# Optimization experiments

Hardware: AMD Instinct MI355X
Metric: run time of the kernel (lower is better)

## Reference

```python
import jax, jax.numpy as jnp
import numpy as np

B, N, M, C, H = 8, 1024, 128, 1024, 16
D = C // H
MLP = int(C * 4.0)
EPS = 1e-6


def setup_inputs() -> dict:
    key = jax.random.key(0)
    ks = jax.random.split(key, 24)
    def w(k, shape):
        return jax.random.normal(k, shape, jnp.float32) * 0.02
    mask = jax.random.randint(ks[3], (B, M), 0, 2, dtype=jnp.int32)
    mask = mask.at[:, 0].set(1)  # ensure at least one attendable token per row
    return {
        "x": jax.random.normal(ks[0], (B, N, C), jnp.float32),
        "c_dino": jax.random.normal(ks[1], (B, C), jnp.float32),
        "c_text": jax.random.normal(ks[2], (B, M, C), jnp.float32),
        "text_mask": mask,
        "W_ada": w(ks[4], (C, 6 * C)), "b_ada": jnp.zeros((6 * C,), jnp.float32),
        "W_qkv": w(ks[5], (C, 3 * C)), "b_qkv": jnp.zeros((3 * C,), jnp.float32),
        "W_proj_sa": w(ks[6], (C, C)), "b_proj_sa": jnp.zeros((C,), jnp.float32),
        "W_q": w(ks[7], (C, C)), "b_q": jnp.zeros((C,), jnp.float32),
        "W_kv": w(ks[8], (C, 2 * C)), "b_kv": jnp.zeros((2 * C,), jnp.float32),
        "W_proj_ca": w(ks[9], (C, C)), "b_proj_ca": jnp.zeros((C,), jnp.float32),
        "W_fc1": w(ks[10], (C, MLP)), "b_fc1": jnp.zeros((MLP,), jnp.float32),
        "W_fc2": w(ks[11], (MLP, C)), "b_fc2": jnp.zeros((C,), jnp.float32),
    }


def _ln(x):
    # LayerNorm without affine params, eps=1e-6
    mu = jnp.mean(x, axis=-1, keepdims=True)
    xc = x - mu
    var = jnp.mean(xc * xc, axis=-1, keepdims=True)
    return xc * jax.lax.rsqrt(var + EPS)


def _modulate(x, shift, scale):
    return x * (1.0 + scale[:, None, :]) + shift[:, None, :]


def _heads(t):
    b, n, _ = t.shape
    return t.reshape(b, n, H, D)


def reference(x, c_dino, c_text, text_mask,
              W_ada, b_ada, W_qkv, b_qkv, W_proj_sa, b_proj_sa,
              W_q, b_q, W_kv, b_kv, W_proj_ca, b_proj_ca,
              W_fc1, b_fc1, W_fc2, b_fc2):
    scale = D ** (-0.5)
    ada = jax.nn.silu(c_dino) @ W_ada + b_ada  # (B, 6C)
    sh_msa, sc_msa, sh_ca, sc_ca, sh_mlp, sc_mlp = jnp.split(ada, 6, axis=1)

    # --- self-attention ---
    h = _modulate(_ln(x), sh_msa, sc_msa)
    qkv = h @ W_qkv + b_qkv
    q, k, v = (_heads(t) for t in jnp.split(qkv, 3, axis=-1))  # (B,N,H,D)
    attn = jax.nn.softmax(jnp.einsum('bnhd,bmhd->bhnm', q, k) * scale, axis=-1)
    sa = jnp.einsum('bhnm,bmhd->bnhd', attn, v).reshape(B, N, C) @ W_proj_sa + b_proj_sa
    x = x + sa

    # --- cross-attention ---
    h = _modulate(_ln(x), sh_ca, sc_ca)
    q = _heads(h @ W_q + b_q)                 # (B,N,H,D)
    kv = c_text @ W_kv + b_kv
    k, v = (_heads(t) for t in jnp.split(kv, 2, axis=-1))  # (B,M,H,D)
    scores = jnp.einsum('bnhd,bmhd->bhnm', q, k) * scale
    scores = jnp.where(text_mask[:, None, None, :] == 0, -jnp.inf, scores)
    attn = jax.nn.softmax(scores, axis=-1)
    ca = jnp.einsum('bhnm,bmhd->bnhd', attn, v).reshape(B, N, C) @ W_proj_ca + b_proj_ca
    x = x + ca

    # --- MLP ---
    h = _modulate(_ln(x), sh_mlp, sc_mlp)
    mlp = jax.nn.gelu(h @ W_fc1 + b_fc1, approximate=True) @ W_fc2 + b_fc2
    return x + mlp
```

## Files before the change

### kernel.cpp

```cpp
#include <hip/hip_runtime.h>
#include <hip/hip_bf16.h>

#define B_   8
#define N_   1024
#define M_   128
#define C_   1024
#define H_   16
#define D_   64
#define MLP_ 4096

typedef __bf16 bf16;
typedef __bf16 bf16x8 __attribute__((ext_vector_type(8)));
typedef __bf16 bf16x4 __attribute__((ext_vector_type(4)));
typedef float  f32x4  __attribute__((ext_vector_type(4)));

__device__ __forceinline__ f32x4 mfma16(bf16x8 a, bf16x8 b, f32x4 c) {
    return __builtin_amdgcn_mfma_f32_16x16x32_bf16(a, b, c, 0, 0, 0);
}

__device__ __forceinline__ void gload16(const bf16* g, bf16* l) {
    __builtin_amdgcn_global_load_lds(
        (const __attribute__((address_space(1))) void*)g,
        (__attribute__((address_space(3))) void*)l, 16, 0, 0);
}

__global__ __launch_bounds__(256) void transpose_k(const float* __restrict__ W,
                                                   bf16* __restrict__ Wt,
                                                   int K, int Nc) {
    __shared__ float tile[32][33];
    const int x  = threadIdx.x & 31;
    const int y0 = threadIdx.x >> 5;
    const size_t n0 = (size_t)blockIdx.x * 32;
    const size_t k0 = (size_t)blockIdx.y * 32;
#pragma unroll
    for (int i = 0; i < 4; i++)
        tile[y0 + i * 8][x] = W[(k0 + y0 + i * 8) * Nc + n0 + x];
    __syncthreads();
#pragma unroll
    for (int i = 0; i < 4; i++)
        Wt[(n0 + y0 + i * 8) * K + k0 + x] = (bf16)tile[x][y0 + i * 8];
}

__global__ __launch_bounds__(256) void cvt_bf16_k(const float* __restrict__ in,
                                                  bf16* __restrict__ out, int n4) {
    int i = blockIdx.x * 256 + threadIdx.x;
    if (i < n4) {
        float4 v = ((const float4*)in)[i];
        bf16x4 o;
        o[0] = (bf16)v.x; o[1] = (bf16)v.y; o[2] = (bf16)v.z; o[3] = (bf16)v.w;
        ((bf16x4*)out)[i] = o;
    }
}

__global__ __launch_bounds__(256) void ada_init_k(const float* __restrict__ bias,
                                                  float* __restrict__ ada) {
    int i = blockIdx.x * 256 + threadIdx.x;
    ada[i] = bias[i % 6144];
}

__global__ __launch_bounds__(256) void ada_k(const float* __restrict__ cdino,
                                             const float* __restrict__ W,
                                             float* __restrict__ ada) {
    __shared__ float sc[8][32];
    const int tid = threadIdx.x;
    const int k0  = blockIdx.y * 32;
    {
        float c = cdino[(tid >> 5) * 1024 + k0 + (tid & 31)];
        sc[tid >> 5][tid & 31] = c / (1.f + __expf(-c));
    }
    __syncthreads();
    const int col = blockIdx.x * 256 + tid;
    float acc[8];
#pragma unroll
    for (int b = 0; b < 8; b++) acc[b] = 0.f;
    for (int kk = 0; kk < 32; kk++) {
        float w = W[(size_t)(k0 + kk) * 6144 + col];
#pragma unroll
        for (int b = 0; b < 8; b++) acc[b] += sc[b][kk] * w;
    }
#pragma unroll
    for (int b = 0; b < 8; b++) atomicAdd(&ada[(size_t)b * 6144 + col], acc[b]);
}

__global__ __launch_bounds__(256) void ln_mod_k(const float* __restrict__ X,
                                                const float* __restrict__ ada,
                                                int shoff, int scoff,
                                                bf16* __restrict__ Hout) {
    const int row = blockIdx.x;
    const int b   = row >> 10;
    const int tid = threadIdx.x;
    const float4 v = ((const float4*)(X + (size_t)row * C_))[tid];
    float s  = v.x + v.y + v.z + v.w;
    float sq = v.x * v.x + v.y * v.y + v.z * v.z + v.w * v.w;
#pragma unroll
    for (int off = 32; off; off >>= 1) {
        s  += __shfl_xor(s,  off);
        sq += __shfl_xor(sq, off);
    }
    __shared__ float rs_[4], rq_[4];
    if ((tid & 63) == 0) { rs_[tid >> 6] = s; rq_[tid >> 6] = sq; }
    __syncthreads();
    s  = rs_[0] + rs_[1] + rs_[2] + rs_[3];
    sq = rq_[0] + rq_[1] + rq_[2] + rq_[3];
    const float mu   = s * (1.f / 1024.f);
    const float var  = sq * (1.f / 1024.f) - mu * mu;
    const float rstd = rsqrtf(var + 1e-6f);
    const float4 scv = ((const float4*)(ada + (size_t)b * 6144 + scoff))[tid];
    const float4 shv = ((const float4*)(ada + (size_t)b * 6144 + shoff))[tid];
    bf16x4 o;
    o[0] = (bf16)(((v.x - mu) * rstd) * (1.f + scv.x) + shv.x);
    o[1] = (bf16)(((v.y - mu) * rstd) * (1.f + scv.y) + shv.y);
    o[2] = (bf16)(((v.z - mu) * rstd) * (1.f + scv.z) + shv.z);
    o[3] = (bf16)(((v.w - mu) * rstd) * (1.f + scv.w) + shv.w);
    *(bf16x4*)(Hout + (size_t)row * C_ + tid * 4) = o;
}

template <int MODE>
__global__ __launch_bounds__(256) void gemm_k(const bf16* __restrict__ A,
                                              const bf16* __restrict__ Bt,
                                              const float* __restrict__ bias,
                                              const float* resid,
                                              float* outF, bf16* outB,
                                              int Ncols, int K) {
    __shared__ __attribute__((aligned(16))) bf16 As[128][32];
    __shared__ __attribute__((aligned(16))) bf16 Bs[128][32];
    const int tid  = threadIdx.x;
    const int lane = tid & 63, wave = tid >> 6;
    const int lrow = lane & 15, quad = lane >> 4;
    const int wm = wave >> 1, wn = wave & 1;
    const size_t bm = (size_t)blockIdx.y * 128;
    const size_t bn = (size_t)blockIdx.x * 128;

    const int srow = tid >> 2, sseg = tid & 3;
    const bf16* gA0 = A  + (bm + srow) * (size_t)K + sseg * 8;
    const bf16* gA1 = gA0 + (size_t)64 * K;
    const bf16* gB0 = Bt + (bn + srow) * (size_t)K + sseg * 8;
    const bf16* gB1 = gB0 + (size_t)64 * K;
    bf16* lA0 = &As[0][0] + wave * 512;
    bf16* lA1 = lA0 + 2048;
    bf16* lB0 = &Bs[0][0] + wave * 512;
    bf16* lB1 = lB0 + 2048;

    f32x4 acc[4][4];
#pragma unroll
    for (int i = 0; i < 4; i++)
#pragma unroll
        for (int j = 0; j < 4; j++) acc[i][j] = (f32x4){0.f, 0.f, 0.f, 0.f};

    for (int ko = 0; ko < K; ko += 32) {
        gload16(gA0 + ko, lA0);
        gload16(gA1 + ko, lA1);
        gload16(gB0 + ko, lB0);
        gload16(gB1 + ko, lB1);
        __syncthreads();
        bf16x8 af[4], bfr[4];
#pragma unroll
        for (int mi = 0; mi < 4; mi++)
            af[mi] = *(const bf16x8*)&As[wm * 64 + mi * 16 + lrow][quad * 8];
#pragma unroll
        for (int ni = 0; ni < 4; ni++)
            bfr[ni] = *(const bf16x8*)&Bs[wn * 64 + ni * 16 + lrow][quad * 8];
#pragma unroll
        for (int mi = 0; mi < 4; mi++)
#pragma unroll
            for (int ni = 0; ni < 4; ni++)
                acc[mi][ni] = mfma16(af[mi], bfr[ni], acc[mi][ni]);
        __syncthreads();
    }

#pragma unroll
    for (int mi = 0; mi < 4; mi++) {
#pragma unroll
        for (int ni = 0; ni < 4; ni++) {
            const size_t gcol = bn + wn * 64 + ni * 16 + lrow;
            const float bv = bias[gcol];
#pragma unroll
            for (int r = 0; r < 4; r++) {
                const size_t grow = bm + wm * 64 + mi * 16 + quad * 4 + r;
                const size_t idx  = grow * Ncols + gcol;
                float v = acc[mi][ni][r] + bv;
                if (MODE == 1) {
                    outF[idx] = v + resid[idx];
                } else if (MODE == 2) {
                    outB[idx] = (bf16)v;
                } else {
                    float z = 1.59576912f * (v + 0.044715f * v * v * v);
                    outB[idx] = (bf16)(v / (1.f + __expf(-z)));
                }
            }
        }
    }
}

template <bool MASKED>
__global__ __launch_bounds__(256) void attn_k(const bf16* __restrict__ Qp, int qstride,
                                              const bf16* __restrict__ KVp, int kvstride,
                                              int koff, int voff,
                                              const int* __restrict__ mask, int Mk,
                                              bf16* __restrict__ O) {
    __shared__ __attribute__((aligned(16))) bf16 Kt[64][88];
    __shared__ __attribute__((aligned(16))) bf16 Vt[64][88];
    __shared__ __attribute__((aligned(16))) bf16 Pt[4][16][88];
    __shared__ float madd[64];

    const int b = blockIdx.z, h = blockIdx.y;
    const int tid  = threadIdx.x;
    const int lane = tid & 63, wave = tid >> 6;
    const int lrow = lane & 15, quad = lane >> 4;
    const int q0 = blockIdx.x * 64 + wave * 16;

    const bf16* qp = Qp + ((size_t)(b * N_ + q0 + lrow)) * qstride + h * 64 + quad * 8;
    const bf16x8 aq0 = *(const bf16x8*)(qp);
    const bf16x8 aq1 = *(const bf16x8*)(qp + 32);

    f32x4 acc[4];
#pragma unroll
    for (int t = 0; t < 4; t++) acc[t] = (f32x4){0.f, 0.f, 0.f, 0.f};
    float mrun[4], lrun[4];
#pragma unroll
    for (int r = 0; r < 4; r++) { mrun[r] = -3e38f; lrun[r] = 0.f; }

    const int skey = tid >> 2;
    const int sd   = (tid & 3) * 16;

    for (int kc = 0; kc < Mk; kc += 64) {
        __syncthreads();
        const bf16* kp = KVp + ((size_t)(b * Mk + kc + skey)) * kvstride + koff + h * 64 + sd;
        bf16x8 k0 = *(const bf16x8*)kp;
        bf16x8 k1 = *(const bf16x8*)(kp + 8);
        *(bf16x8*)&Kt[skey][sd]     = k0;
        *(bf16x8*)&Kt[skey][sd + 8] = k1;
        const bf16* vp = KVp + ((size_t)(b * Mk + kc + skey)) * kvstride + voff + h * 64 + sd;
        bf16x8 v0 = *(const bf16x8*)vp;
        bf16x8 v1 = *(const bf16x8*)(vp + 8);
#pragma unroll
        for (int i = 0; i < 8; i++) Vt[sd + i][skey] = v0[i];
#pragma unroll
        for (int i = 0; i < 8; i++) Vt[sd + 8 + i][skey] = v1[i];
        if (MASKED && tid < 64)
            madd[tid] = (mask[b * Mk + kc + tid] == 0) ? -1e30f : 0.f;
        __syncthreads();

        float sv[4][4];
#pragma unroll
        for (int t = 0; t < 4; t++) {
            f32x4 s = (f32x4){0.f, 0.f, 0.f, 0.f};
            bf16x8 bk0 = *(const bf16x8*)&Kt[t * 16 + lrow][quad * 8];
            s = mfma16(aq0, bk0, s);
            bf16x8 bk1 = *(const bf16x8*)&Kt[t * 16 + lrow][32 + quad * 8];
            s = mfma16(aq1, bk1, s);
            const float ma = MASKED ? madd[t * 16 + lrow] : 0.f;
#pragma unroll
            for (int r = 0; r < 4; r++) sv[t][r] = s[r] * 0.125f + ma;
        }

        float pv[4][4], alpha[4];
#pragma unroll
        for (int r = 0; r < 4; r++) {
            float vmax = fmaxf(fmaxf(sv[0][r], sv[1][r]), fmaxf(sv[2][r], sv[3][r]));
#pragma unroll
            for (int off = 1; off < 16; off <<= 1) vmax = fmaxf(vmax, __shfl_xor(vmax, off));
            const float mnew = fmaxf(mrun[r], vmax);
            alpha[r] = __expf(mrun[r] - mnew);
            mrun[r] = mnew;
            float rsum = 0.f;
#pragma unroll
            for (int t = 0; t < 4; t++) {
                float p = __expf(sv[t][r] - mnew);
                pv[t][r] = p;
                rsum += p;
            }
#pragma unroll
            for (int off = 1; off < 16; off <<= 1) rsum += __shfl_xor(rsum, off);
            lrun[r] = lrun[r] * alpha[r] + rsum;
        }
#pragma unroll
        for (int t = 0; t < 4; t++)
#pragma unroll
            for (int r = 0; r < 4; r++) acc[t][r] *= alpha[r];

#pragma unroll
        for (int t = 0; t < 4; t++)
#pragma unroll
            for (int r = 0; r < 4; r++)
                Pt[wave][quad * 4 + r][t * 16 + lrow] = (bf16)pv[t][r];
        __syncthreads();
        const bf16x8 ap0 = *(const bf16x8*)&Pt[wave][lrow][quad * 8];
        const bf16x8 ap1 = *(const bf16x8*)&Pt[wave][lrow][32 + quad * 8];

#pragma unroll
        for (int t = 0; t < 4; t++) {
            bf16x8 bv0 = *(const bf16x8*)&Vt[t * 16 + lrow][quad * 8];
            acc[t] = mfma16(ap0, bv0, acc[t]);
            bf16x8 bv1 = *(const bf16x8*)&Vt[t * 16 + lrow][32 + quad * 8];
            acc[t] = mfma16(ap1, bv1, acc[t]);
        }
    }

#pragma unroll
    for (int r = 0; r < 4; r++) {
        const float inv = 1.f / lrun[r];
        const size_t grow = (size_t)(b * N_ + q0 + quad * 4 + r);
#pragma unroll
        for (int t = 0; t < 4; t++)
            O[grow * C_ + h * 64 + t * 16 + lrow] = (bf16)(acc[t][r] * inv);
    }
}

extern "C" void kernel_launch(void* const* d_in, const int* in_sizes, int n_in,
                              void* d_out, int out_size, void* d_ws, size_t ws_size,
                              hipStream_t stream) {
    const float* x     = (const float*)d_in[0];
    const float* cdino = (const float*)d_in[1];
    const float* ctext = (const float*)d_in[2];
    const int*   tmask = (const int*)d_in[3];
    const float* W_ada = (const float*)d_in[4];
    const float* b_ada = (const float*)d_in[5];
    const float* W_qkv = (const float*)d_in[6];
    const float* b_qkv = (const float*)d_in[7];
    const float* W_sa  = (const float*)d_in[8];
    const float* b_sa  = (const float*)d_in[9];
    const float* W_q   = (const float*)d_in[10];
    const float* b_q   = (const float*)d_in[11];
    const float* W_kv  = (const float*)d_in[12];
    const float* b_kv  = (const float*)d_in[13];
    const float* W_ca  = (const float*)d_in[14];
    const float* b_ca  = (const float*)d_in[15];
    const float* W_fc1 = (const float*)d_in[16];
    const float* b_fc1 = (const float*)d_in[17];
    const float* W_fc2 = (const float*)d_in[18];
    const float* b_fc2 = (const float*)d_in[19];
    float* out = (float*)d_out;

    char* ws = (char*)d_ws;
    size_t off = 0;
    auto alloc = [&](size_t bytes) -> char* {
        char* p = ws + off;
        off += (bytes + 255) & ~(size_t)255;
        return p;
    };
    float* ada  = (float*)alloc((size_t)8 * 6144 * 4);
    bf16* ctxb  = (bf16*)alloc((size_t)1024 * 1024 * 2);
    bf16* WqkvT = (bf16*)alloc((size_t)3072 * 1024 * 2);
    bf16* WsaT  = (bf16*)alloc((size_t)1024 * 1024 * 2);
    bf16* WqT   = (bf16*)alloc((size_t)1024 * 1024 * 2);
    bf16* WkvT  = (bf16*)alloc((size_t)2048 * 1024 * 2);
    bf16* WcaT  = (bf16*)alloc((size_t)1024 * 1024 * 2);
    bf16* Wfc1T = (bf16*)alloc((size_t)4096 * 1024 * 2);
    bf16* Wfc2T = (bf16*)alloc((size_t)1024 * 4096 * 2);
    float* xbuf = (float*)alloc((size_t)8192 * 1024 * 4);
    bf16* hbuf  = (bf16*)alloc((size_t)8192 * 1024 * 2);
    bf16* attnb = (bf16*)alloc((size_t)8192 * 1024 * 2);
    bf16* pool  = (bf16*)alloc((size_t)8192 * 4096 * 2);
    if (off > ws_size) return;

    bf16* qkvb  = pool;
    bf16* qb    = pool;
    bf16* kvb   = pool + (size_t)8192 * 1024;
    bf16* gelub = pool;

    transpose_k<<<dim3(3072 / 32, 1024 / 32), 256, 0, stream>>>(W_qkv, WqkvT, 1024, 3072);
    transpose_k<<<dim3(1024 / 32, 1024 / 32), 256, 0, stream>>>(W_sa,  WsaT,  1024, 1024);
    transpose_k<<<dim3(1024 / 32, 1024 / 32), 256, 0, stream>>>(W_q,   WqT,   1024, 1024);
    transpose_k<<<dim3(2048 / 32, 1024 / 32), 256, 0, stream>>>(W_kv,  WkvT,  1024, 2048);
    transpose_k<<<dim3(1024 / 32, 1024 / 32), 256, 0, stream>>>(W_ca,  WcaT,  1024, 1024);
    transpose_k<<<dim3(4096 / 32, 1024 / 32), 256, 0, stream>>>(W_fc1, Wfc1T, 1024, 4096);
    transpose_k<<<dim3(1024 / 32, 4096 / 32), 256, 0, stream>>>(W_fc2, Wfc2T, 4096, 1024);
    cvt_bf16_k<<<1024, 256, 0, stream>>>(ctext, ctxb, 262144);

    ada_init_k<<<192, 256, 0, stream>>>(b_ada, ada);
    ada_k<<<dim3(24, 32), 256, 0, stream>>>(cdino, W_ada, ada);

    ln_mod_k<<<8192, 256, 0, stream>>>(x, ada, 0, 1024, hbuf);
    gemm_k<2><<<dim3(24, 64), 256, 0, stream>>>(hbuf, WqkvT, b_qkv, nullptr, nullptr, qkvb, 3072, 1024);
    attn_k<false><<<dim3(16, 16, 8), 256, 0, stream>>>(qkvb, 3072, qkvb, 3072, 1024, 2048,
                                                       nullptr, 1024, attnb);
    gemm_k<1><<<dim3(8, 64), 256, 0, stream>>>(attnb, WsaT, b_sa, x, xbuf, nullptr, 1024, 1024);

    ln_mod_k<<<8192, 256, 0, stream>>>(xbuf, ada, 2048, 3072, hbuf);
    gemm_k<2><<<dim3(8, 64), 256, 0, stream>>>(hbuf, WqT, b_q, nullptr, nullptr, qb, 1024, 1024);
    gemm_k<2><<<dim3(16, 8), 256, 0, stream>>>(ctxb, WkvT, b_kv, nullptr, nullptr, kvb, 2048, 1024);
    attn_k<true><<<dim3(16, 16, 8), 256, 0, stream>>>(qb, 1024, kvb, 2048, 0, 1024,
                                                      tmask, 128, attnb);
    gemm_k<1><<<dim3(8, 64), 256, 0, stream>>>(attnb, WcaT, b_ca, xbuf, xbuf, nullptr, 1024, 1024);

    ln_mod_k<<<8192, 256, 0, stream>>>(xbuf, ada, 4096, 5120, hbuf);
    gemm_k<3><<<dim3(32, 64), 256, 0, stream>>>(hbuf, Wfc1T, b_fc1, nullptr, nullptr, gelub, 4096, 1024);
    gemm_k<1><<<dim3(8, 64), 256, 0, stream>>>(gelub, Wfc2T, b_fc2, xbuf, out, nullptr, 1024, 4096);
}
```

Baseline: 825.3 us.

## Pre-transpose V in global memory and compute transposed scores in attention

Adds a separate kernel that transposes V per batch into a head-dim-major global buffer, so the attention kernel can stage V into shared memory with vector stores instead of scattered scalar transposing writes. The score MFMA is also swapped to compute K·Q^T. Each lane then holds one query's scores across four rows, which shrinks the row max and sum reductions to two cross-lane shuffles. Probabilities are written to shared memory as packed bf16x4. This costs extra launches and an additional global write and read of V, in exchange for cheaper shared-memory staging and softmax inside attention.

```diff
diff --git a/kernel.cpp b/kernel.cpp
--- a/kernel.cpp
+++ b/kernel.cpp
@@ -39,6 +39,23 @@
 #pragma unroll
     for (int i = 0; i < 4; i++)
         Wt[(n0 + y0 + i * 8) * K + k0 + x] = (bf16)tile[x][y0 + i * 8];
+}
+
+__global__ __launch_bounds__(256) void vtrans_k(const bf16* __restrict__ in, int instride,
+                                                int coff, int Mk, bf16* __restrict__ outT) {
+    __shared__ bf16 t[32][33];
+    const int tx = threadIdx.x & 31;
+    const int ty0 = threadIdx.x >> 5;
+    const int m0  = blockIdx.x * 32;
+    const int hd0 = blockIdx.y * 32;
+    const int b   = blockIdx.z;
+#pragma unroll
+    for (int i = 0; i < 4; i++)
+        t[ty0 + i * 8][tx] = in[((size_t)(b * Mk + m0 + ty0 + i * 8)) * instride + coff + hd0 + tx];
+    __syncthreads();
+#pragma unroll
+    for (int i = 0; i < 4; i++)
+        outT[((size_t)(b * 1024 + hd0 + ty0 + i * 8)) * Mk + m0 + tx] = t[tx][ty0 + i * 8];
 }
 
 __global__ __launch_bounds__(256) void cvt_bf16_k(const float* __restrict__ in,
@@ -194,8 +211,8 @@
 
 template <bool MASKED>
 __global__ __launch_bounds__(256) void attn_k(const bf16* __restrict__ Qp, int qstride,
-                                              const bf16* __restrict__ KVp, int kvstride,
-                                              int koff, int voff,
+                                              const bf16* __restrict__ Kp, int kstride,
+                                              const bf16* __restrict__ Vtg,
                                               const int* __restrict__ mask, int Mk,
                                               bf16* __restrict__ O) {
     __shared__ __attribute__((aligned(16))) bf16 Kt[64][88];
@@ -210,33 +227,32 @@
     const int q0 = blockIdx.x * 64 + wave * 16;
 
     const bf16* qp = Qp + ((size_t)(b * N_ + q0 + lrow)) * qstride + h * 64 + quad * 8;
-    const bf16x8 aq0 = *(const bf16x8*)(qp);
-    const bf16x8 aq1 = *(const bf16x8*)(qp + 32);
+    const bf16x8 bq0 = *(const bf16x8*)(qp);
+    const bf16x8 bq1 = *(const bf16x8*)(qp + 32);
 
     f32x4 acc[4];
 #pragma unroll
     for (int t = 0; t < 4; t++) acc[t] = (f32x4){0.f, 0.f, 0.f, 0.f};
-    float mrun[4], lrun[4];
-#pragma unroll
-    for (int r = 0; r < 4; r++) { mrun[r] = -3e38f; lrun[r] = 0.f; }
-
-    const int skey = tid >> 2;
-    const int sd   = (tid & 3) * 16;
+    float mrun = -3e38f, lrun = 0.f;
+
+    const int srow = tid >> 2;
+    const int sseg = (tid & 3) * 16;
+
+    const bf16* kbase = Kp + ((size_t)b * Mk + srow) * kstride + h * 64 + sseg;
+    const bf16* vbase = Vtg + ((size_t)(b * 1024 + h * 64 + srow)) * Mk + sseg;
 
     for (int kc = 0; kc < Mk; kc += 64) {
         __syncthreads();
-        const bf16* kp = KVp + ((size_t)(b * Mk + kc + skey)) * kvstride + koff + h * 64 + sd;
+        const bf16* kp = kbase + (size_t)kc * kstride;
         bf16x8 k0 = *(const bf16x8*)kp;
         bf16x8 k1 = *(const bf16x8*)(kp + 8);
-        *(bf16x8*)&Kt[skey][sd]     = k0;
-        *(bf16x8*)&Kt[skey][sd + 8] = k1;
-        const bf16* vp = KVp + ((size_t)(b * Mk + kc + skey)) * kvstride + voff + h * 64 + sd;
+        *(bf16x8*)&Kt[srow][sseg]     = k0;
+        *(bf16x8*)&Kt[srow][sseg + 8] = k1;
+        const bf16* vp = vbase + kc;
         bf16x8 v0 = *(const bf16x8*)vp;
         bf16x8 v1 = *(const bf16x8*)(vp + 8);
-#pragma unroll
-        for (int i = 0; i < 8; i++) Vt[sd + i][skey] = v0[i];
-#pragma unroll
-        for (int i = 0; i < 8; i++) Vt[sd + 8 + i][skey] = v1[i];
+        *(bf16x8*)&Vt[srow][sseg]     = v0;
+        *(bf16x8*)&Vt[srow][sseg + 8] = v1;
         if (MASKED && tid < 64)
             madd[tid] = (mask[b * Mk + kc + tid] == 0) ? -1e30f : 0.f;
         __syncthreads();
@@ -245,45 +261,51 @@
 #pragma unroll
         for (int t = 0; t < 4; t++) {
             f32x4 s = (f32x4){0.f, 0.f, 0.f, 0.f};
-            bf16x8 bk0 = *(const bf16x8*)&Kt[t * 16 + lrow][quad * 8];
-            s = mfma16(aq0, bk0, s);
-            bf16x8 bk1 = *(const bf16x8*)&Kt[t * 16 + lrow][32 + quad * 8];
-            s = mfma16(aq1, bk1, s);
-            const float ma = MASKED ? madd[t * 16 + lrow] : 0.f;
-#pragma unroll
-            for (int r = 0; r < 4; r++) sv[t][r] = s[r] * 0.125f + ma;
+            bf16x8 ak0 = *(const bf16x8*)&Kt[t * 16 + lrow][quad * 8];
+            s = mfma16(ak0, bq0, s);
+            bf16x8 ak1 = *(const bf16x8*)&Kt[t * 16 + lrow][32 + quad * 8];
+            s = mfma16(ak1, bq1, s);
+#pragma unroll
+            for (int r = 0; r < 4; r++) {
+                float ma = MASKED ? madd[t * 16 + quad * 4 + r] : 0.f;
+                sv[t][r] = s[r] * 0.125f + ma;
+            }
         }
 
-        float pv[4][4], alpha[4];
-#pragma unroll
-        for (int r = 0; r < 4; r++) {
-            float vmax = fmaxf(fmaxf(sv[0][r], sv[1][r]), fmaxf(sv[2][r], sv[3][r]));
-#pragma unroll
-            for (int off = 1; off < 16; off <<= 1) vmax = fmaxf(vmax, __shfl_xor(vmax, off));
-            const float mnew = fmaxf(mrun[r], vmax);
-            alpha[r] = __expf(mrun[r] - mnew);
-            mrun[r] = mnew;
-            float rsum = 0.f;
-#pragma unroll
-            for (int t = 0; t < 4; t++) {
+        float vmax = sv[0][0];
+#pragma unroll
+        for (int t = 0; t < 4; t++)
+#pragma unroll
+            for (int r = 0; r < 4; r++) vmax = fmaxf(vmax, sv[t][r]);
+        vmax = fmaxf(vmax, __shfl_xor(vmax, 16));
+        vmax = fmaxf(vmax, __shfl_xor(vmax, 32));
+        const float mnew  = fmaxf(mrun, vmax);
+        const float alpha = __expf(mrun - mnew);
+        mrun = mnew;
+        float rsum = 0.f;
+#pragma unroll
+        for (int t = 0; t < 4; t++) {
+            bf16x4 p4;
+#pragma unroll
+            for (int r = 0; r < 4; r++) {
                 float p = __expf(sv[t][r] - mnew);
-                pv[t][r] = p;
                 rsum += p;
+                p4[r] = (bf16)p;
             }
-#pragma unroll
-            for (int off = 1; off < 16; off <<= 1) rsum += __shfl_xor(rsum, off);
-            lrun[r] = lrun[r] * alpha[r] + rsum;
+            *(bf16x4*)&Pt[wave][lrow][t * 16 + quad * 4] = p4;
         }
+        rsum += __shfl_xor(rsum, 16);
+        rsum += __shfl_xor(rsum, 32);
+        lrun = lrun * alpha + rsum;
+
+        float alpha4[4];
+#pragma unroll
+        for (int r = 0; r < 4; r++) alpha4[r] = __shfl(alpha, quad * 4 + r);
 #pragma unroll
         for (int t = 0; t < 4; t++)
 #pragma unroll
-            for (int r = 0; r < 4; r++) acc[t][r] *= alpha[r];
-
-#pragma unroll
-        for (int t = 0; t < 4; t++)
-#pragma unroll
-            for (int r = 0; r < 4; r++)
-                Pt[wave][quad * 4 + r][t * 16 + lrow] = (bf16)pv[t][r];
+            for (int r = 0; r < 4; r++) acc[t][r] *= alpha4[r];
+
         __syncthreads();
         const bf16x8 ap0 = *(const bf16x8*)&Pt[wave][lrow][quad * 8];
         const bf16x8 ap1 = *(const bf16x8*)&Pt[wave][lrow][32 + quad * 8];
@@ -297,13 +319,16 @@
         }
     }
 
+    float linv = 1.f / lrun;
+    float linv4[4];
+#pragma unroll
+    for (int r = 0; r < 4; r++) linv4[r] = __shfl(linv, quad * 4 + r);
 #pragma unroll
     for (int r = 0; r < 4; r++) {
-        const float inv = 1.f / lrun[r];
         const size_t grow = (size_t)(b * N_ + q0 + quad * 4 + r);
 #pragma unroll
         for (int t = 0; t < 4; t++)
-            O[grow * C_ + h * 64 + t * 16 + lrow] = (bf16)(acc[t][r] * inv);
+            O[grow * C_ + h * 64 + t * 16 + lrow] = (bf16)(acc[t][r] * linv4[r]);
     }
 }
 
@@ -351,6 +376,8 @@
     float* xbuf = (float*)alloc((size_t)8192 * 1024 * 4);
     bf16* hbuf  = (bf16*)alloc((size_t)8192 * 1024 * 2);
     bf16* attnb = (bf16*)alloc((size_t)8192 * 1024 * 2);
+    bf16* VtgSA = (bf16*)alloc((size_t)8192 * 1024 * 2);
+    bf16* VtgCA = (bf16*)alloc((size_t)8192 * 128 * 2);
     bf16* pool  = (bf16*)alloc((size_t)8192 * 4096 * 2);
     if (off > ws_size) return;
 
@@ -373,14 +400,16 @@
 
     ln_mod_k<<<8192, 256, 0, stream>>>(x, ada, 0, 1024, hbuf);
     gemm_k<2><<<dim3(24, 64), 256, 0, stream>>>(hbuf, WqkvT, b_qkv, nullptr, nullptr, qkvb, 3072, 1024);
-    attn_k<false><<<dim3(16, 16, 8), 256, 0, stream>>>(qkvb, 3072, qkvb, 3072, 1024, 2048,
+    vtrans_k<<<dim3(32, 32, 8), 256, 0, stream>>>(qkvb, 3072, 2048, 1024, VtgSA);
+    attn_k<false><<<dim3(16, 16, 8), 256, 0, stream>>>(qkvb, 3072, qkvb + 1024, 3072, VtgSA,
                                                        nullptr, 1024, attnb);
     gemm_k<1><<<dim3(8, 64), 256, 0, stream>>>(attnb, WsaT, b_sa, x, xbuf, nullptr, 1024, 1024);
 
     ln_mod_k<<<8192, 256, 0, stream>>>(xbuf, ada, 2048, 3072, hbuf);
     gemm_k<2><<<dim3(8, 64), 256, 0, stream>>>(hbuf, WqT, b_q, nullptr, nullptr, qb, 1024, 1024);
     gemm_k<2><<<dim3(16, 8), 256, 0, stream>>>(ctxb, WkvT, b_kv, nullptr, nullptr, kvb, 2048, 1024);
-    attn_k<true><<<dim3(16, 16, 8), 256, 0, stream>>>(qb, 1024, kvb, 2048, 0, 1024,
+    vtrans_k<<<dim3(4, 32, 8), 256, 0, stream>>>(kvb, 2048, 1024, 128, VtgCA);
+    attn_k<true><<<dim3(16, 16, 8), 256, 0, stream>>>(qb, 1024, kvb, 2048, VtgCA,
                                                       tmask, 128, attnb);
     gemm_k<1><<<dim3(8, 64), 256, 0, stream>>>(attnb, WcaT, b_ca, xbuf, xbuf, nullptr, 1024, 1024);
 
```

Measured after the change: 790.7 us. 1.04x faster.
